# Optimization experiments

Hardware: AMD Instinct MI355X
Metric: run time of the kernel (lower is better)

The kernel has to match this reference:

```python
import jax, jax.numpy as jnp
import numpy as np
from jax import lax

V = 100000       # vocab_size / num_words
E = 300          # embedding_size (== num_units, required by compare stage)
M = 300          # num_units / mem_dim
NC = 3           # num_classes
L = 128          # leaves per tree -> N = 2L-1 nodes
N = 2 * L - 1


def build_tree(num_leaves):
    # balanced binary tree, postorder node numbering (children before parent)
    left, right = [], []
    def rec(lo, hi):
        if hi - lo == 1:
            left.append(-1); right.append(-1)
            return len(left) - 1
        mid = (lo + hi) // 2
        l = rec(lo, mid)
        r = rec(mid, hi)
        left.append(l); right.append(r)
        return len(left) - 1
    rec(0, num_leaves)
    return np.asarray(left, np.int32), np.asarray(right, np.int32)


def setup_inputs() -> dict:
    key = jax.random.key(0)
    ks = jax.random.split(key, 20)
    l1, r1 = build_tree(L)
    l2, r2 = build_tree(L)
    s = 0.1  # param scale (stands in for orthogonal init)
    inp = {
        "sent1": jax.random.randint(ks[0], (N,), 0, V),
        "sent2": jax.random.randint(ks[1], (N,), 0, V),
        "left1": jnp.asarray(l1), "right1": jnp.asarray(r1),
        "left2": jnp.asarray(l2), "right2": jnp.asarray(r2),
        "emb": jax.random.normal(ks[2], (V, E), jnp.float32),
        # composer x-projections, gate order: [cx, ix, fx, ox]
        "Wx_i": jax.random.normal(ks[3], (4, M, E), jnp.float32) * s,
        "bx_i": jnp.zeros((4, M), jnp.float32),
        # composer h-projections, gate order: [u, i, lf, rf, o]
        "Wl_i": jax.random.normal(ks[4], (5, M, M), jnp.float32) * s,
        "Wr_i": jax.random.normal(ks[5], (5, M, M), jnp.float32) * s,
        "Wx_c": jax.random.normal(ks[6], (4, M, M), jnp.float32) * s,
        "bx_c": jnp.zeros((4, M), jnp.float32),
        "Wl_c": jax.random.normal(ks[7], (5, M, M), jnp.float32) * s,
        "Wr_c": jax.random.normal(ks[8], (5, M, M), jnp.float32) * s,
        "Wc": jax.random.normal(ks[9], (M, 4 * M), jnp.float32) * 0.01,
        "bc": jnp.zeros((M,), jnp.float32),
        "Wa1": jax.random.normal(ks[10], (M, 4 * M), jnp.float32) * 0.01,
        "ba1": jnp.zeros((M,), jnp.float32),
        "Wa2": jax.random.normal(ks[11], (NC, M), jnp.float32) * 0.01,
        "ba2": jnp.zeros((NC,), jnp.float32),
    }
    return inp


def tree_lstm(xg, left, right, Wl, Wr):
    # xg: [N, 4, M] precomputed x-gate terms (cx, ix, fx, ox)
    # Wl/Wr: [5, M, M] hidden-state gate weights (u, i, lf, rf, o)
    n, _, m = xg.shape
    zero = jnp.zeros((m,), xg.dtype)

    def step(carry, t):
        C, H = carry
        i, l, r = t
        lc = jnp.where(l >= 0, C[jnp.maximum(l, 0)], zero)
        lh = jnp.where(l >= 0, H[jnp.maximum(l, 0)], zero)
        rc = jnp.where(r >= 0, C[jnp.maximum(r, 0)], zero)
        rh = jnp.where(r >= 0, H[jnp.maximum(r, 0)], zero)
        gl = jnp.einsum('gmd,d->gm', Wl, lh)  # [5, M]
        gr = jnp.einsum('gmd,d->gm', Wr, rh)
        x = xg[i]  # [4, M]
        u  = jnp.tanh(x[0] + gl[0] + gr[0])
        ig = jax.nn.sigmoid(x[1] + gl[1] + gr[1])
        lf = jax.nn.sigmoid(x[2] + gl[2] + gr[2])  # fx shared for both forgets (as in source)
        rf = jax.nn.sigmoid(x[2] + gl[3] + gr[3])
        c = ig * u + lf * lc + rf * rc
        o = jax.nn.sigmoid(x[3] + gl[4] + gr[4])
        h = o * jnp.tanh(c)
        return (C.at[i].set(c), H.at[i].set(h)), None

    init = (jnp.zeros((n, m), xg.dtype), jnp.zeros((n, m), xg.dtype))
    (_, H), _ = lax.scan(step, init, (jnp.arange(n), left, right))
    return H  # [N, M] all node hidden states in postorder


def reference(sent1, sent2, left1, right1, left2, right2, emb,
              Wx_i, bx_i, Wl_i, Wr_i, Wx_c, bx_c, Wl_c, Wr_c,
              Wc, bc, Wa1, ba1, Wa2, ba2):
    pad = emb.shape[0] - 1  # num_words - 1

    def encode(sent, left, right):
        # leaves embed their token; internal nodes embed PAD (PAD=True path)
        tok = jnp.where(left < 0, sent, pad)
        x = emb[tok]                                        # [N, E]
        xg = jnp.einsum('nd,gmd->ngm', x, Wx_i) + bx_i      # [N, 4, M]
        return tree_lstm(xg, left, right, Wl_i, Wr_i)

    s1 = encode(sent1, left1, right1)  # [N1, M]
    s2 = encode(sent2, left2, right2)  # [N2, M]

    raw = s1 @ s2.T                                         # [N1, N2]
    beta = jax.nn.softmax(raw, axis=1) @ s2                 # aligned to s1
    alpha = jax.nn.softmax(raw.T, axis=1) @ s1              # aligned to s2

    def compare(s, a, left, right):
        feat = jnp.concatenate([s, a, s - a, s * a], axis=-1)  # [N, 4M]
        h = jax.nn.relu(feat @ Wc.T + bc)                      # [N, M]
        xg = jnp.einsum('nd,gmd->ngm', h, Wx_c) + bx_c
        return tree_lstm(xg, left, right, Wl_c, Wr_c)

    v1 = compare(s1, beta, left1, right1)
    v2 = compare(s2, alpha, left2, right2)

    agg = jnp.concatenate([v1.mean(0), v1.max(0), v2.mean(0), v2.max(0)])  # [4M]
    hidden = jax.nn.relu(agg @ Wa1.T + ba1)
    logits = hidden @ Wa2.T + ba2
    return logits[None, :]  # [1, num_classes]
```

## Files before the change

kernel.cpp:

```cpp
#include <hip/hip_runtime.h>
#include <math.h>

#define NN 255
#define TC 510
#define HTLD 512

typedef unsigned int uint32;

__device__ __forceinline__ float sigm(float x){ return 1.f/(1.f+expf(-x)); }

__device__ __forceinline__ float aload(const float* p){ return __hip_atomic_load(p, __ATOMIC_RELAXED, __HIP_MEMORY_SCOPE_AGENT); }
__device__ __forceinline__ void astore(float* p, float v){ __hip_atomic_store(p, v, __ATOMIC_RELAXED, __HIP_MEMORY_SCOPE_AGENT); }
__device__ __forceinline__ uint32 aloadu(const uint32* p){ return __hip_atomic_load(p, __ATOMIC_RELAXED, __HIP_MEMORY_SCOPE_AGENT); }

__device__ __forceinline__ void leaf_gate(const float* __restrict__ xgp, int m, float& c, float& h){
  float x0 = xgp[m], x1 = xgp[300+m], x3 = xgp[900+m];
  float u = tanhf(x0), ig = sigm(x1);
  c = ig * u;
  h = sigm(x3) * tanhf(c);
}

__global__ __launch_bounds__(512) void k_setup(const int* __restrict__ l1, const int* __restrict__ r1,
                                               const int* __restrict__ l2, const int* __restrict__ r2,
                                               int4* __restrict__ lists2, int* __restrict__ cnt)
{
  __shared__ int lv[TC];
  __shared__ int cs[16];
  int t = threadIdx.x;
  if (t < TC) lv[t] = 0;
  if (t < 16) cs[t] = 0;
  __syncthreads();
  for (int it = 0; it < 12; ++it){
    int nv = 0;
    if (t < TC){
      int tr = t >= NN, i = t - tr * NN;
      const int* L = tr ? l2 : l1;
      const int* R = tr ? r2 : r1;
      int l = L[i], r = R[i];
      nv = (l < 0) ? 0 : 1 + max(lv[tr * NN + l], lv[tr * NN + r]);
    }
    __syncthreads();
    if (t < TC) lv[t] = nv;
    __syncthreads();
  }
  if (t < TC){
    int tr = t >= NN, i = t - tr * NN;
    int v = min(lv[t], 15);
    int pos = atomicAdd(&cs[v], 1);
    int l = (tr ? l2 : l1)[i], r = (tr ? r2 : r1)[i];
    lists2[v * 256 + pos] = make_int4(tr * NN + i, tr * NN + max(l, 0), tr * NN + max(r, 0), 0);
  }
  __syncthreads();
  if (t < 16) cnt[t] = cs[t];
}

template<int NG>
__global__ __launch_bounds__(256, 3) void k_tree(
    const float* __restrict__ Wl, const float* __restrict__ Wr,
    const float* __restrict__ xg,
    float* __restrict__ H, float* __restrict__ C, float* __restrict__ HT,
    const int4* __restrict__ lists2, const int* __restrict__ cnt,
    uint32* __restrict__ rdy)
{
  constexpr int NB = NG * 75;
  __shared__ float Hs[16][2][320];
  __shared__ float Cs[16][4][2];
  __shared__ float Xs[16][4][4];
  __shared__ int4 nfo[512];
  __shared__ int lvoff[9];

  const int tid = threadIdx.x;
  const int lane = tid & 63, team = tid >> 6;
  const int mblk = blockIdx.x % 75, grp = blockIdx.x / 75;
  const int m = mblk * 4 + team;

  float wl[5][5], wr[5][5];
  #pragma unroll
  for (int g = 0; g < 5; ++g)
    #pragma unroll
    for (int j = 0; j < 5; ++j){
      int d = j * 64 + lane;
      size_t o = ((size_t)g * 300 + m) * 300 + d;
      wl[g][j] = (d < 300) ? Wl[o] : 0.f;
      wr[g][j] = (d < 300) ? Wr[o] : 0.f;
    }

  if (tid == 0){ lvoff[0] = 0; for (int lv = 1; lv <= 7; ++lv) lvoff[lv] = lvoff[lv-1] + cnt[lv-1]; }
  __syncthreads();
  for (int lv = 0; lv <= 7; ++lv)
    for (int i = tid; i < cnt[lv]; i += 256)
      nfo[lvoff[lv] + i] = lists2[lv * 256 + i];
  __syncthreads();

  {
    int nodes = cnt[0];
    int npg = (nodes + NG - 1) / NG;
    int n0 = grp * npg, n1 = min(nodes, n0 + npg);
    for (int nb0 = n0; nb0 < n1; nb0 += 64){
      int nch = min(64, n1 - nb0);
      if (tid < nch * 4){
        int ni = tid >> 2, tm = tid & 3;
        int gi = nfo[nb0 + ni].x;
        int mm = mblk * 4 + tm;
        float c, h; leaf_gate(xg + (size_t)gi * 1200, mm, c, h);
        astore(&C[(size_t)gi * 300 + mm], c);
        astore(&H[(size_t)gi * 300 + mm], h);
        astore(&HT[(size_t)mm * HTLD + gi], h);
      }
      asm volatile("s_waitcnt vmcnt(0)" ::: "memory");
      __syncthreads();
      if (tid < nch) atomicAdd(&rdy[nfo[nb0 + tid].x], 1u);
    }
  }

  for (int lv = 1; lv <= 7; ++lv){
    int nodes = cnt[lv];
    int npg = (nodes + NG - 1) / NG;
    int n0 = grp * npg, n1 = min(nodes, n0 + npg);
    for (int nb0 = n0; nb0 < n1; nb0 += 16){
      int nch = min(16, n1 - nb0);
      int base = lvoff[lv] + nb0;
      __syncthreads();
      if (tid < nch){
        int4 nn = nfo[base + tid];
        while (aloadu(&rdy[nn.y]) < 75u) __builtin_amdgcn_s_sleep(8);
        while (aloadu(&rdy[nn.z]) < 75u) __builtin_amdgcn_s_sleep(8);
      }
      __syncthreads();
      #pragma unroll
      for (int p = 0; p < 2; ++p){
        int niA = team + p * 8, niB = niA + 4;
        bool vA = niA < nch, vB = niB < nch;
        int4 na = vA ? nfo[base + niA] : make_int4(0, 0, 0, 0);
        int4 nb4 = vB ? nfo[base + niB] : make_int4(0, 0, 0, 0);
        int d0 = lane, d1 = 64 + lane, d2 = 128 + lane, d3 = 192 + lane, d4 = 256 + lane;
        bool i4 = d4 < 300;
        #define LDH(ci, dd, ok) ((ok) ? aload(&H[(size_t)(ci) * 300 + (dd)]) : 0.f)
        float a0=LDH(na.y,d0,vA), a1=LDH(na.y,d1,vA), a2=LDH(na.y,d2,vA), a3=LDH(na.y,d3,vA), a4=LDH(na.y,d4,vA&&i4);
        float a5=LDH(na.z,d0,vA), a6=LDH(na.z,d1,vA), a7=LDH(na.z,d2,vA), a8=LDH(na.z,d3,vA), a9=LDH(na.z,d4,vA&&i4);
        float c0=LDH(nb4.y,d0,vB), c1=LDH(nb4.y,d1,vB), c2=LDH(nb4.y,d2,vB), c3=LDH(nb4.y,d3,vB), c4=LDH(nb4.y,d4,vB&&i4);
        float c5=LDH(nb4.z,d0,vB), c6=LDH(nb4.z,d1,vB), c7=LDH(nb4.z,d2,vB), c8=LDH(nb4.z,d3,vB), c9=LDH(nb4.z,d4,vB&&i4);
        #undef LDH
        if (vA){
          Hs[niA][0][d0]=a0; Hs[niA][0][d1]=a1; Hs[niA][0][d2]=a2; Hs[niA][0][d3]=a3; Hs[niA][0][d4]=a4;
          Hs[niA][1][d0]=a5; Hs[niA][1][d1]=a6; Hs[niA][1][d2]=a7; Hs[niA][1][d3]=a8; Hs[niA][1][d4]=a9;
        }
        if (vB){
          Hs[niB][0][d0]=c0; Hs[niB][0][d1]=c1; Hs[niB][0][d2]=c2; Hs[niB][0][d3]=c3; Hs[niB][0][d4]=c4;
          Hs[niB][1][d0]=c5; Hs[niB][1][d1]=c6; Hs[niB][1][d2]=c7; Hs[niB][1][d3]=c8; Hs[niB][1][d4]=c9;
        }
      }
      if (tid < 128){
        int ni = tid >> 3, tm = (tid >> 1) & 3, side = tid & 1;
        if (ni < nch){
          int4 nn = nfo[base + ni];
          int child = side ? nn.z : nn.y;
          Cs[ni][tm][side] = aload(&C[(size_t)child * 300 + mblk * 4 + tm]);
        }
      }
      {
        int ni = tid >> 4, tm = (tid >> 2) & 3, g = tid & 3;
        if (ni < nch){
          int4 nn = nfo[base + ni];
          Xs[ni][tm][g] = xg[(size_t)nn.x * 1200 + g * 300 + mblk * 4 + tm];
        }
      }
      __syncthreads();
      #pragma unroll 2
      for (int ni = 0; ni < nch; ++ni){
        float p0 = 0.f, p1 = 0.f, p2 = 0.f, p3 = 0.f, p4 = 0.f;
        #pragma unroll
        for (int j = 0; j < 5; ++j){
          float hl = Hs[ni][0][j * 64 + lane];
          float hr = Hs[ni][1][j * 64 + lane];
          p0 += wl[0][j] * hl + wr[0][j] * hr;
          p1 += wl[1][j] * hl + wr[1][j] * hr;
          p2 += wl[2][j] * hl + wr[2][j] * hr;
          p3 += wl[3][j] * hl + wr[3][j] * hr;
          p4 += wl[4][j] * hl + wr[4][j] * hr;
        }
        #pragma unroll
        for (int off = 32; off; off >>= 1){
          p0 += __shfl_xor(p0, off); p1 += __shfl_xor(p1, off); p2 += __shfl_xor(p2, off);
          p3 += __shfl_xor(p3, off); p4 += __shfl_xor(p4, off);
        }
        if (lane == 0){
          int4 nn = nfo[base + ni];
          int gi = nn.x;
          float lc = Cs[ni][team][0], rc = Cs[ni][team][1];
          float u  = tanhf(Xs[ni][team][0] + p0);
          float ig = sigm (Xs[ni][team][1] + p1);
          float lf = sigm (Xs[ni][team][2] + p2);
          float rf = sigm (Xs[ni][team][2] + p3);
          float o  = sigm (Xs[ni][team][3] + p4);
          float cc = ig * u + lf * lc + rf * rc;
          float hv = o * tanhf(cc);
          astore(&C[(size_t)gi * 300 + m], cc);
          astore(&H[(size_t)gi * 300 + m], hv);
          astore(&HT[(size_t)m * HTLD + gi], hv);
        }
      }
      asm volatile("s_waitcnt vmcnt(0)" ::: "memory");
      __syncthreads();
      if (tid < nch) atomicAdd(&rdy[nfo[base + tid].x], 1u);
    }
  }
}

__global__ __launch_bounds__(256) void k_xg(const int* __restrict__ sent1, const int* __restrict__ sent2,
                                            const int* __restrict__ l1, const int* __restrict__ l2,
                                            const float* __restrict__ emb, int pad,
                                            const float* __restrict__ W, const float* __restrict__ bias,
                                            const float* __restrict__ hsrc, float* __restrict__ out)
{
  __shared__ float Z[8][300];
  int tx = threadIdx.x, ty = threadIdx.y;
  int t = ty * 64 + tx;
  int colbase = blockIdx.y * 8;
  for (int c = 0; c < 8; ++c){
    int gcol = colbase + c;
    if (gcol < TC){
      if (hsrc){
        for (int k = t; k < 300; k += 256) Z[c][k] = hsrc[(size_t)gcol * 300 + k];
      } else {
        int tr = gcol >= NN, node = gcol - tr * NN;
        int tok = ((tr ? l2 : l1)[node] < 0) ? (tr ? sent2 : sent1)[node] : pad;
        const float* e = emb + (size_t)tok * 300;
        for (int k = t; k < 300; k += 256) Z[c][k] = e[k];
      }
    } else {
      for (int k = t; k < 300; k += 256) Z[c][k] = 0.f;
    }
  }
  __syncthreads();
  int r = blockIdx.x * 64 + tx;
  if (r < 1200){
    float a0 = 0.f, a1 = 0.f;
    const float* wp = W + (size_t)r * 300;
    for (int k = 0; k < 300; k += 4){
      float4 wv = *(const float4*)(wp + k);
      float4 z0 = *(const float4*)(&Z[ty][k]);
      float4 z1 = *(const float4*)(&Z[ty + 4][k]);
      a0 += wv.x*z0.x + wv.y*z0.y + wv.z*z0.z + wv.w*z0.w;
      a1 += wv.x*z1.x + wv.y*z1.y + wv.z*z1.z + wv.w*z1.w;
    }
    float b = bias[r];
    int g0 = colbase + ty, g1 = colbase + ty + 4;
    if (g0 < TC) out[(size_t)g0 * 1200 + r] = a0 + b;
    if (g1 < TC) out[(size_t)g1 * 1200 + r] = a1 + b;
  }
}

__global__ __launch_bounds__(256) void k_attn2(const float* __restrict__ H, const float* __restrict__ HT,
                                               float* __restrict__ ab)
{
  __shared__ float q[4][304];
  __shared__ float S[4][256];
  __shared__ float red[256];
  __shared__ float invs[4];
  int t = threadIdx.x;
  int dir = blockIdx.x >= 64;
  int r0 = (blockIdx.x - dir * 64) * 4;
  int nr = min(4, NN - r0);
  const float* Ss = H + (dir ? (size_t)NN * 300 : 0);
  const float* So = H + (dir ? 0 : (size_t)NN * 300);
  int oppb = dir ? 0 : NN;

  for (int idx = t; idx < 4 * 304; idx += 256){
    int r = idx / 304, k = idx - r * 304;
    q[r][k] = (r < nr && k < 300) ? Ss[(size_t)(r0 + r) * 300 + k] : 0.f;
  }
  __syncthreads();

  float s0 = 0.f, s1 = 0.f, s2 = 0.f, s3 = 0.f;
  if (t < NN){
    const float* hp = HT + oppb + t;
    #pragma unroll 4
    for (int k = 0; k < 300; ++k){
      float ht = hp[(size_t)k * HTLD];
      s0 += q[0][k] * ht; s1 += q[1][k] * ht; s2 += q[2][k] * ht; s3 += q[3][k] * ht;
    }
  }
  S[0][t] = (t < NN) ? s0 : -1e30f;
  S[1][t] = (t < NN) ? s1 : -1e30f;
  S[2][t] = (t < NN) ? s2 : -1e30f;
  S[3][t] = (t < NN) ? s3 : -1e30f;
  __syncthreads();

  for (int r = 0; r < nr; ++r){
    red[t] = S[r][t];
    __syncthreads();
    for (int s = 128; s; s >>= 1){ if (t < s) red[t] = fmaxf(red[t], red[t + s]); __syncthreads(); }
    float mx = red[0];
    __syncthreads();
    float e = (t < NN) ? expf(S[r][t] - mx) : 0.f;
    S[r][t] = e;
    red[t] = e;
    __syncthreads();
    for (int s = 128; s; s >>= 1){ if (t < s) red[t] += red[t + s]; __syncthreads(); }
    if (t == 0) invs[r] = 1.f / red[0];
    __syncthreads();
  }

  float a0=0,a1=0,a2=0,a3=0, b0=0,b1=0,b2=0,b3=0;
  int m2 = t + 256;
  bool has2 = m2 < 300;
  for (int j = 0; j < NN; ++j){
    const float* sp = So + (size_t)j * 300;
    float v1 = (t < 300) ? sp[t] : 0.f;
    float v2 = has2 ? sp[m2] : 0.f;
    float p0 = S[0][j], p1 = S[1][j], p2 = S[2][j], p3 = S[3][j];
    a0 += p0 * v1; a1 += p1 * v1; a2 += p2 * v1; a3 += p3 * v1;
    b0 += p0 * v2; b1 += p1 * v2; b2 += p2 * v2; b3 += p3 * v2;
  }
  float accs1[4] = {a0, a1, a2, a3};
  float accs2[4] = {b0, b1, b2, b3};
  for (int r = 0; r < nr; ++r){
    size_t rowo = (size_t)(dir * NN + r0 + r) * 300;
    if (t < 300) ab[rowo + t] = accs1[r] * invs[r];
    if (has2)    ab[rowo + m2] = accs2[r] * invs[r];
  }
}

__global__ __launch_bounds__(256) void k_hcmp(const float* __restrict__ Henc, const float* __restrict__ ab,
                                              const float* __restrict__ Wc, const float* __restrict__ bc,
                                              float* __restrict__ hc)
{
  __shared__ float Z[8][1200];
  int tx = threadIdx.x, ty = threadIdx.y;
  int t = ty * 64 + tx;
  int colbase = blockIdx.y * 8;
  for (int c = 0; c < 8; ++c){
    int gcol = colbase + c;
    if (gcol < TC){
      const float* sp = Henc + (size_t)gcol * 300;
      const float* ap = ab + (size_t)gcol * 300;
      for (int k = t; k < 1200; k += 256){
        int sel = k >= 900 ? 3 : (k >= 600 ? 2 : (k >= 300 ? 1 : 0));
        int kk = k - sel * 300;
        float s = sp[kk], a = ap[kk];
        Z[c][k] = sel == 0 ? s : sel == 1 ? a : sel == 2 ? (s - a) : (s * a);
      }
    } else {
      for (int k = t; k < 1200; k += 256) Z[c][k] = 0.f;
    }
  }
  __syncthreads();
  int r = blockIdx.x * 64 + tx;
  if (r < 300){
    float a0 = 0.f, a1 = 0.f;
    const float* wp = Wc + (size_t)r * 1200;
    for (int k = 0; k < 1200; k += 4){
      float4 wv = *(const float4*)(wp + k);
      float4 z0 = *(const float4*)(&Z[ty][k]);
      float4 z1 = *(const float4*)(&Z[ty + 4][k]);
      a0 += wv.x*z0.x + wv.y*z0.y + wv.z*z0.z + wv.w*z0.w;
      a1 += wv.x*z1.x + wv.y*z1.y + wv.z*z1.z + wv.w*z1.w;
    }
    float b = bc[r];
    int g0 = colbase + ty, g1 = colbase + ty + 4;
    if (g0 < TC) hc[(size_t)g0 * 300 + r] = fmaxf(a0 + b, 0.f);
    if (g1 < TC) hc[(size_t)g1 * 300 + r] = fmaxf(a1 + b, 0.f);
  }
}

__global__ __launch_bounds__(256) void k_agg(const float* __restrict__ HTc, float* __restrict__ agg)
{
  __shared__ float red[256];
  int idx = blockIdx.x;
  int tr = idx / 300, m = idx - tr * 300;
  int t = threadIdx.x;
  const float* p = HTc + (size_t)m * HTLD + tr * NN;
  float v = (t < NN) ? p[t] : 0.f;
  red[t] = v;
  __syncthreads();
  for (int s = 128; s; s >>= 1){ if (t < s) red[t] += red[t + s]; __syncthreads(); }
  float sum = red[0];
  __syncthreads();
  red[t] = (t < NN) ? v : -1e30f;
  __syncthreads();
  for (int s = 128; s; s >>= 1){ if (t < s) red[t] = fmaxf(red[t], red[t + s]); __syncthreads(); }
  if (t == 0){
    agg[tr * 600 + m] = sum / 255.f;
    agg[tr * 600 + 300 + m] = red[0];
  }
}

__global__ __launch_bounds__(256) void k_mlp1(const float* __restrict__ agg,
                                              const float* __restrict__ Wa1, const float* __restrict__ ba1,
                                              float* __restrict__ hid)
{
  __shared__ float red[256];
  int h = blockIdx.x, t = threadIdx.x;
  const float* wp = Wa1 + (size_t)h * 1200;
  float a = 0.f;
  for (int k = t; k < 1200; k += 256) a += wp[k] * agg[k];
  red[t] = a;
  __syncthreads();
  for (int s = 128; s; s >>= 1){ if (t < s) red[t] += red[t + s]; __syncthreads(); }
  if (t == 0) hid[h] = fmaxf(red[0] + ba1[h], 0.f);
}

__global__ __launch_bounds__(256) void k_mlp2(const float* __restrict__ hid,
                                              const float* __restrict__ Wa2, const float* __restrict__ ba2,
                                              float* __restrict__ out)
{
  __shared__ float h_s[300];
  int t = threadIdx.x;
  for (int k = t; k < 300; k += 256) h_s[k] = hid[k];
  __syncthreads();
  if (t < 192){
    int c = t >> 6, ln = t & 63;
    float a = 0.f;
    for (int k = ln; k < 300; k += 64) a += Wa2[c * 300 + k] * h_s[k];
    #pragma unroll
    for (int off = 32; off; off >>= 1) a += __shfl_down(a, off);
    if (ln == 0) out[c] = a + ba2[c];
  }
}

extern "C" void kernel_launch(void* const* d_in, const int* in_sizes, int n_in,
                              void* d_out, int out_size, void* d_ws, size_t ws_size,
                              hipStream_t stream)
{
  const int*   sent1 = (const int*)d_in[0];
  const int*   sent2 = (const int*)d_in[1];
  const int*   l1    = (const int*)d_in[2];
  const int*   r1    = (const int*)d_in[3];
  const int*   l2    = (const int*)d_in[4];
  const int*   r2    = (const int*)d_in[5];
  const float* emb   = (const float*)d_in[6];
  const float* Wx_i  = (const float*)d_in[7];
  const float* bx_i  = (const float*)d_in[8];
  const float* Wl_i  = (const float*)d_in[9];
  const float* Wr_i  = (const float*)d_in[10];
  const float* Wx_c  = (const float*)d_in[11];
  const float* bx_c  = (const float*)d_in[12];
  const float* Wl_c  = (const float*)d_in[13];
  const float* Wr_c  = (const float*)d_in[14];
  const float* Wcm   = (const float*)d_in[15];
  const float* bcm   = (const float*)d_in[16];
  const float* Wa1   = (const float*)d_in[17];
  const float* ba1   = (const float*)d_in[18];
  const float* Wa2   = (const float*)d_in[19];
  const float* ba2   = (const float*)d_in[20];
  int V = in_sizes[6] / 300;
  int pad = V - 1;

  char* w = (char*)d_ws;
  uint32* rdy1   = (uint32*)w;
  uint32* rdy2   = (uint32*)(w + 4096);
  int*    cnt    = (int*)(w + 8192);
  int4*   lists2 = (int4*)(w + 8256);
  float* xg   = (float*)(w + 8256 + 65536);
  float* Henc = xg + 612000;
  float* Hcmp = Henc + 153000;
  float* C    = Hcmp + 153000;
  float* ab   = C + 153000;
  float* hc   = ab + 153000;
  float* HTe  = hc + 153000;
  float* HTc  = HTe + 153600;
  float* agg  = HTc + 153600;
  float* hid  = agg + 1200;
  float* outp = (float*)d_out;

  hipMemsetAsync(rdy1, 0, 8192, stream);

  int nb6 = 0, nCU = 0;
  hipError_t eq = hipOccupancyMaxActiveBlocksPerMultiprocessor(&nb6, reinterpret_cast<const void*>(&k_tree<8>), 256, 0);
  hipError_t ec = hipDeviceGetAttribute(&nCU, hipDeviceAttributeMultiprocessorCount, 0);
  bool ok600 = (eq == hipSuccess) && (ec == hipSuccess) && (nb6 * nCU >= 600);

  k_setup<<<1, 512, 0, stream>>>(l1, r1, l2, r2, lists2, cnt);
  dim3 blk(64, 4);

  k_xg<<<dim3(19, 64), blk, 0, stream>>>(sent1, sent2, l1, l2, emb, pad, Wx_i, bx_i, nullptr, xg);
  {
    void* args[] = {(void*)&Wl_i, (void*)&Wr_i, (void*)&xg,
                    (void*)&Henc, (void*)&C, (void*)&HTe, (void*)&lists2, (void*)&cnt, (void*)&rdy1};
    if (ok600) hipLaunchCooperativeKernel((void*)&k_tree<8>, dim3(600), dim3(256), args, 0, stream);
    else       hipLaunchCooperativeKernel((void*)&k_tree<4>, dim3(300), dim3(256), args, 0, stream);
  }

  k_attn2<<<128, 256, 0, stream>>>(Henc, HTe, ab);

  k_hcmp<<<dim3(5, 64), blk, 0, stream>>>(Henc, ab, Wcm, bcm, hc);
  k_xg<<<dim3(19, 64), blk, 0, stream>>>(sent1, sent2, l1, l2, emb, pad, Wx_c, bx_c, hc, xg);
  {
    void* args[] = {(void*)&Wl_c, (void*)&Wr_c, (void*)&xg,
                    (void*)&Hcmp, (void*)&C, (void*)&HTc, (void*)&lists2, (void*)&cnt, (void*)&rdy2};
    if (ok600) hipLaunchCooperativeKernel((void*)&k_tree<8>, dim3(600), dim3(256), args, 0, stream);
    else       hipLaunchCooperativeKernel((void*)&k_tree<4>, dim3(300), dim3(256), args, 0, stream);
  }

  k_agg<<<600, 256, 0, stream>>>(HTc, agg);
  k_mlp1<<<300, 256, 0, stream>>>(agg, Wa1, ba1, hid);
  k_mlp2<<<1, 256, 0, stream>>>(hid, Wa2, ba2, outp);
}
```

Measured before the change: 489.4 us.

## Pad ready counters to cache lines and compute pad-token projection once

Each ready counter now sits in its own 128-byte slot (index shifted by 5), so different nodes' spin-waits and atomics no longer share a cache line, and the spin sleep interval is halved. In the encoder pass, internal nodes all use the pad token, so the x-projection is computed only for leaves plus one extra pad row. The tree kernel reads that shared row for internal nodes. This skips most of the first k_xg matmul's stores and embedding gathers, but it enlarges the workspace and the memset of the ready counters.

After: 490.1 us. No clear change (+0.1%).

```diff
diff --git a/kernel.cpp b/kernel.cpp
--- a/kernel.cpp
+++ b/kernel.cpp
@@ -4,6 +4,7 @@
 #define NN 255
 #define TC 510
 #define HTLD 512
+#define RSH 5
 
 typedef unsigned int uint32;
 
@@ -57,7 +58,7 @@
 template<int NG>
 __global__ __launch_bounds__(256, 3) void k_tree(
     const float* __restrict__ Wl, const float* __restrict__ Wr,
-    const float* __restrict__ xg,
+    const float* __restrict__ xg, int xrow,
     float* __restrict__ H, float* __restrict__ C, float* __restrict__ HT,
     const int4* __restrict__ lists2, const int* __restrict__ cnt,
     uint32* __restrict__ rdy)
@@ -109,7 +110,7 @@
       }
       asm volatile("s_waitcnt vmcnt(0)" ::: "memory");
       __syncthreads();
-      if (tid < nch) atomicAdd(&rdy[nfo[nb0 + tid].x], 1u);
+      if (tid < nch) atomicAdd(&rdy[(uint32)nfo[nb0 + tid].x << RSH], 1u);
     }
   }
 
@@ -123,8 +124,8 @@
       __syncthreads();
       if (tid < nch){
         int4 nn = nfo[base + tid];
-        while (aloadu(&rdy[nn.y]) < 75u) __builtin_amdgcn_s_sleep(8);
-        while (aloadu(&rdy[nn.z]) < 75u) __builtin_amdgcn_s_sleep(8);
+        while (aloadu(&rdy[(uint32)nn.y << RSH]) < 75u) __builtin_amdgcn_s_sleep(4);
+        while (aloadu(&rdy[(uint32)nn.z << RSH]) < 75u) __builtin_amdgcn_s_sleep(4);
       }
       __syncthreads();
       #pragma unroll
@@ -161,8 +162,8 @@
       {
         int ni = tid >> 4, tm = (tid >> 2) & 3, g = tid & 3;
         if (ni < nch){
-          int4 nn = nfo[base + ni];
-          Xs[ni][tm][g] = xg[(size_t)nn.x * 1200 + g * 300 + mblk * 4 + tm];
+          int row = (xrow >= 0) ? xrow : nfo[base + ni].x;
+          Xs[ni][tm][g] = xg[(size_t)row * 1200 + g * 300 + mblk * 4 + tm];
         }
       }
       __syncthreads();
@@ -202,7 +203,7 @@
       }
       asm volatile("s_waitcnt vmcnt(0)" ::: "memory");
       __syncthreads();
-      if (tid < nch) atomicAdd(&rdy[nfo[base + tid].x], 1u);
+      if (tid < nch) atomicAdd(&rdy[(uint32)nfo[base + tid].x << RSH], 1u);
     }
   }
 }
@@ -214,17 +215,33 @@
                                             const float* __restrict__ hsrc, float* __restrict__ out)
 {
   __shared__ float Z[8][300];
+  __shared__ int wr_s[8];
   int tx = threadIdx.x, ty = threadIdx.y;
   int t = ty * 64 + tx;
   int colbase = blockIdx.y * 8;
+  if (t < 8){
+    int gcol = colbase + t;
+    int w = 0;
+    if (hsrc) w = (gcol < TC) ? 1 : 0;
+    else {
+      if (gcol == TC) w = 1;
+      else if (gcol < TC){
+        int tr = gcol >= NN, node = gcol - tr * NN;
+        w = ((tr ? l2 : l1)[node] < 0) ? 1 : 0;
+      }
+    }
+    wr_s[t] = w;
+  }
+  __syncthreads();
   for (int c = 0; c < 8; ++c){
     int gcol = colbase + c;
-    if (gcol < TC){
+    if (wr_s[c]){
       if (hsrc){
         for (int k = t; k < 300; k += 256) Z[c][k] = hsrc[(size_t)gcol * 300 + k];
       } else {
-        int tr = gcol >= NN, node = gcol - tr * NN;
-        int tok = ((tr ? l2 : l1)[node] < 0) ? (tr ? sent2 : sent1)[node] : pad;
+        int tok;
+        if (gcol == TC) tok = pad;
+        else { int tr = gcol >= NN; tok = (tr ? sent2 : sent1)[gcol - tr * NN]; }
         const float* e = emb + (size_t)tok * 300;
         for (int k = t; k < 300; k += 256) Z[c][k] = e[k];
       }
@@ -246,8 +263,8 @@
     }
     float b = bias[r];
     int g0 = colbase + ty, g1 = colbase + ty + 4;
-    if (g0 < TC) out[(size_t)g0 * 1200 + r] = a0 + b;
-    if (g1 < TC) out[(size_t)g1 * 1200 + r] = a1 + b;
+    if (g0 <= TC && wr_s[ty])     out[(size_t)g0 * 1200 + r] = a0 + b;
+    if (g1 <= TC && wr_s[ty + 4]) out[(size_t)g1 * 1200 + r] = a1 + b;
   }
 }
 
@@ -449,11 +466,11 @@
 
   char* w = (char*)d_ws;
   uint32* rdy1   = (uint32*)w;
-  uint32* rdy2   = (uint32*)(w + 4096);
-  int*    cnt    = (int*)(w + 8192);
-  int4*   lists2 = (int4*)(w + 8256);
-  float* xg   = (float*)(w + 8256 + 65536);
-  float* Henc = xg + 612000;
+  uint32* rdy2   = (uint32*)(w + 65536);
+  int*    cnt    = (int*)(w + 131072);
+  int4*   lists2 = (int4*)(w + 131136);
+  float* xg   = (float*)(w + 131136 + 65536);
+  float* Henc = xg + 613200;
   float* Hcmp = Henc + 153000;
   float* C    = Hcmp + 153000;
   float* ab   = C + 153000;
@@ -464,7 +481,7 @@
   float* hid  = agg + 1200;
   float* outp = (float*)d_out;
 
-  hipMemsetAsync(rdy1, 0, 8192, stream);
+  hipMemsetAsync(rdy1, 0, 131072, stream);
 
   int nb6 = 0, nCU = 0;
   hipError_t eq = hipOccupancyMaxActiveBlocksPerMultiprocessor(&nb6, reinterpret_cast<const void*>(&k_tree<8>), 256, 0);
@@ -473,10 +490,12 @@
 
   k_setup<<<1, 512, 0, stream>>>(l1, r1, l2, r2, lists2, cnt);
   dim3 blk(64, 4);
+  int padRow = TC;
+  int ownRow = -1;
 
   k_xg<<<dim3(19, 64), blk, 0, stream>>>(sent1, sent2, l1, l2, emb, pad, Wx_i, bx_i, nullptr, xg);
   {
-    void* args[] = {(void*)&Wl_i, (void*)&Wr_i, (void*)&xg,
+    void* args[] = {(void*)&Wl_i, (void*)&Wr_i, (void*)&xg, (void*)&padRow,
                     (void*)&Henc, (void*)&C, (void*)&HTe, (void*)&lists2, (void*)&cnt, (void*)&rdy1};
     if (ok600) hipLaunchCooperativeKernel((void*)&k_tree<8>, dim3(600), dim3(256), args, 0, stream);
     else       hipLaunchCooperativeKernel((void*)&k_tree<4>, dim3(300), dim3(256), args, 0, stream);
@@ -487,7 +506,7 @@
   k_hcmp<<<dim3(5, 64), blk, 0, stream>>>(Henc, ab, Wcm, bcm, hc);
   k_xg<<<dim3(19, 64), blk, 0, stream>>>(sent1, sent2, l1, l2, emb, pad, Wx_c, bx_c, hc, xg);
   {
-    void* args[] = {(void*)&Wl_c, (void*)&Wr_c, (void*)&xg,
+    void* args[] = {(void*)&Wl_c, (void*)&Wr_c, (void*)&xg, (void*)&ownRow,
                     (void*)&Hcmp, (void*)&C, (void*)&HTc, (void*)&lists2, (void*)&cnt, (void*)&rdy2};
     if (ok600) hipLaunchCooperativeKernel((void*)&k_tree<8>, dim3(600), dim3(256), args, 0, stream);
     else       hipLaunchCooperativeKernel((void*)&k_tree<4>, dim3(300), dim3(256), args, 0, stream);
```
